# Optimization experiments

Measured on AMD Instinct MI355X. Metric: run time of the kernel, lower is better.

Reference implementation:

```python
import math
import jax, jax.numpy as jnp
import numpy as np

N = 100000
F_IN = 256
H = 64
D = 16          # dim_latent
C = 8           # n_classes
L = 10          # radial_layers
K = 10          # APPNP steps
ALPHA = 0.1
BETA_PRIOR = 0.001
E = 3200000
BN_EPS = 1e-5
LOG_SCALE = 0.5 * D * math.log(4 * math.pi)


def setup_inputs() -> dict:
    key = jax.random.key(0)
    ks = jax.random.split(key, 16)
    x = jax.random.normal(ks[0], (N, F_IN), dtype=jnp.float32)
    edge_index = jax.random.randint(ks[1], (2, E), 0, N, dtype=jnp.int64)
    s1 = 1.0 / math.sqrt(F_IN)
    s2 = 1.0 / math.sqrt(H)
    return {
        'x': x,
        'edge_index': edge_index,
        'W1': jax.random.uniform(ks[2], (F_IN, H), jnp.float32, -s1, s1),
        'b1': jnp.zeros((H,), jnp.float32),
        'g1': jnp.ones((H,), jnp.float32),
        'be1': jnp.zeros((H,), jnp.float32),
        'W2': jax.random.uniform(ks[3], (H, H), jnp.float32, -s2, s2),
        'b2': jnp.zeros((H,), jnp.float32),
        'g2': jnp.ones((H,), jnp.float32),
        'be2': jnp.zeros((H,), jnp.float32),
        'W3': jax.random.uniform(ks[4], (H, D), jnp.float32, -s2, s2),
        'b3': jnp.zeros((D,), jnp.float32),
        # flow params: per layer l, per class c
        'x0': jax.random.normal(ks[5], (L, C, D), jnp.float32) * 0.1,
        'alpha_prime': jnp.zeros((L, C), jnp.float32),
        'beta_prime': jnp.zeros((L, C), jnp.float32),
        'mu': jnp.zeros((C, D), jnp.float32),
        'log_var': jnp.zeros((C, D), jnp.float32),
    }


def _batchnorm(h, g, b):
    m = h.mean(axis=0)
    v = h.var(axis=0)  # biased, as torch BN training forward
    return g * (h - m) / jnp.sqrt(v + BN_EPS) + b


def _flow_log_prob(z, x0, alpha_prime, beta_prime, mu, log_var):
    # z: [N, D] -> log q(z|c): [N, C]. Dropout off (eval); loop over L=10 layers.
    zz = jnp.broadcast_to(z[:, None, :], (z.shape[0], C, D))  # [N,C,D]
    log_det = jnp.zeros((z.shape[0], C), z.dtype)
    for l in reversed(range(L)):  # reversed(transforms)
        a = jax.nn.softplus(alpha_prime[l])[None, :, None]      # [1,C,1]
        b = -a + jax.nn.softplus(beta_prime[l])[None, :, None]
        diff = zz - x0[l][None]                                  # [N,C,D]
        r = jnp.maximum(jnp.linalg.norm(diff, axis=-1, keepdims=True), 1e-8)
        h = 1.0 / (a + r)
        zz = zz + b * h * diff
        h_prime = -1.0 / (a + r) ** 2
        log_det = log_det + (D - 1) * jnp.log1p(b * h)[..., 0] \
                  + jnp.log1p(b * h + b * h_prime * r)[..., 0]
    var = jnp.exp(log_var)  # [C,D]
    log_p_base = (-0.5 * D * math.log(2 * math.pi)
                  - 0.5 * log_var.sum(axis=-1)[None, :]
                  - 0.5 * ((zz - mu[None]) ** 2 / var[None]).sum(axis=-1))
    return log_p_base + log_det  # [N,C]


def _appnp(beta_ft, row, col, n_nodes):
    e = row.shape[0]
    deg = jax.ops.segment_sum(jnp.ones((e,), beta_ft.dtype), row, num_segments=n_nodes)
    dis = jnp.where(deg > 0, deg ** -0.5, 0.0)
    norm = dis[row] * dis[col]  # [E']
    h = beta_ft
    for _ in range(K):
        msg = jax.ops.segment_sum(norm[:, None] * h[col], row, num_segments=n_nodes)
        h = (1.0 - ALPHA) * msg + ALPHA * beta_ft
    return h


def reference(x, edge_index, W1, b1, g1, be1, W2, b2, g2, be2, W3, b3,
              x0, alpha_prime, beta_prime, mu, log_var):
    n = x.shape[0]
    # encoder (BN in batch-stats mode, dropout disabled)
    h1 = jax.nn.relu(_batchnorm(x @ W1 + b1, g1, be1))
    h2 = jax.nn.relu(_batchnorm(h1 @ W2 + b2, g2, be2))
    z = h2 @ W3 + b3  # [N,D]
    log_q = _flow_log_prob(z, x0, alpha_prime, beta_prime, mu, log_var)  # [N,C]
    beta_ft = jnp.exp(jnp.clip(log_q + LOG_SCALE, -30.0, 30.0))
    # add self loops
    sl = jnp.arange(n, dtype=edge_index.dtype)
    row = jnp.concatenate([edge_index[0], sl])
    col = jnp.concatenate([edge_index[1], sl])
    beta_agg = _appnp(beta_ft, row, col, n)
    alpha = BETA_PRIOR + jnp.maximum(beta_agg, 0.0)
    probs = alpha / alpha.sum(axis=-1, keepdims=True)
    return alpha, probs, z, beta_ft, log_q
```

## Files before the change

kernel.cpp:

```cpp
#include <hip/hip_runtime.h>

#define NFEAT_IN 256
#define HDIM 64
#define DLAT 16
#define NC 8
#define NL 10
#define KPROP 10
#define ELLW 64
#define OVF_CAP 8192
#define NB 128
#define PERTHREAD 16
#define TILE (256 * PERTHREAD)
#define BM 64
#define BKT 64

__device__ __forceinline__ float softplusf(float x) {
    return (x > 20.f) ? x : log1pf(expf(x));
}

__global__ __launch_bounds__(256) void k_gemm1(
        const float* __restrict__ x, const float* __restrict__ W1,
        const float* __restrict__ b1, float* __restrict__ t1t, int n) {
    __shared__ float xs[BKT][BM + 4];
    __shared__ float ws[BKT][HDIM];
    int t = threadIdx.x;
    int row0 = blockIdx.x * BM;
    int tr = t >> 4, tc = t & 15;
    float acc[4][4];
    float4 bv = *reinterpret_cast<const float4*>(&b1[tc * 4]);
    #pragma unroll
    for (int i = 0; i < 4; ++i) {
        acc[i][0] = bv.x; acc[i][1] = bv.y; acc[i][2] = bv.z; acc[i][3] = bv.w;
    }
    for (int k0 = 0; k0 < NFEAT_IN; k0 += BKT) {
        __syncthreads();
        #pragma unroll
        for (int it = 0; it < 4; ++it) {
            int i = it * 256 + t;
            int row = i >> 4, q = i & 15;
            int grow = row0 + row;
            float4 v = make_float4(0.f, 0.f, 0.f, 0.f);
            if (grow < n)
                v = *reinterpret_cast<const float4*>(
                        &x[(size_t)grow * NFEAT_IN + k0 + q * 4]);
            xs[q * 4 + 0][row] = v.x;
            xs[q * 4 + 1][row] = v.y;
            xs[q * 4 + 2][row] = v.z;
            xs[q * 4 + 3][row] = v.w;
        }
        #pragma unroll
        for (int it = 0; it < 4; ++it) {
            int i = it * 256 + t;
            int kk = i >> 4, q = i & 15;
            *reinterpret_cast<float4*>(&ws[kk][q * 4]) =
                *reinterpret_cast<const float4*>(&W1[(size_t)(k0 + kk) * HDIM + q * 4]);
        }
        __syncthreads();
        #pragma unroll 8
        for (int kk = 0; kk < BKT; ++kk) {
            float4 a = *reinterpret_cast<const float4*>(&xs[kk][tr * 4]);
            float4 w = *reinterpret_cast<const float4*>(&ws[kk][tc * 4]);
            acc[0][0] += a.x * w.x; acc[0][1] += a.x * w.y;
            acc[0][2] += a.x * w.z; acc[0][3] += a.x * w.w;
            acc[1][0] += a.y * w.x; acc[1][1] += a.y * w.y;
            acc[1][2] += a.y * w.z; acc[1][3] += a.y * w.w;
            acc[2][0] += a.z * w.x; acc[2][1] += a.z * w.y;
            acc[2][2] += a.z * w.z; acc[2][3] += a.z * w.w;
            acc[3][0] += a.w * w.x; acc[3][1] += a.w * w.y;
            acc[3][2] += a.w * w.z; acc[3][3] += a.w * w.w;
        }
    }
    int r = row0 + tr * 4;
    if (r < n) {
        #pragma unroll
        for (int cj = 0; cj < 4; ++cj) {
            int j = tc * 4 + cj;
            float4 v = make_float4(acc[0][cj], acc[1][cj], acc[2][cj], acc[3][cj]);
            *reinterpret_cast<float4*>(&t1t[(size_t)j * n + r]) = v;
        }
    }
}

__global__ __launch_bounds__(256) void k_gemm2(
        const float* __restrict__ t1t, const float* __restrict__ A1,
        const float* __restrict__ B1, const float* __restrict__ W2,
        const float* __restrict__ b2, float* __restrict__ t2t, int n) {
    __shared__ float xs[HDIM][BM + 4];
    __shared__ float ws[HDIM][HDIM];
    __shared__ float As[HDIM], Bs[HDIM];
    int t = threadIdx.x;
    int row0 = blockIdx.x * BM;
    if (t < HDIM) { As[t] = A1[t]; Bs[t] = B1[t]; }
    __syncthreads();
    int tr = t >> 4, tc = t & 15;
    #pragma unroll
    for (int it = 0; it < 4; ++it) {
        int i = it * 256 + t;
        int kk = i >> 4, q = i & 15;
        float4 v = make_float4(0.f, 0.f, 0.f, 0.f);
        if (row0 + q * 4 < n) {
            v = *reinterpret_cast<const float4*>(&t1t[(size_t)kk * n + row0 + q * 4]);
            float a = As[kk], b = Bs[kk];
            v.x = fmaxf(fmaf(a, v.x, b), 0.f);
            v.y = fmaxf(fmaf(a, v.y, b), 0.f);
            v.z = fmaxf(fmaf(a, v.z, b), 0.f);
            v.w = fmaxf(fmaf(a, v.w, b), 0.f);
        }
        *reinterpret_cast<float4*>(&xs[kk][q * 4]) = v;
    }
    #pragma unroll
    for (int it = 0; it < 4; ++it) {
        int i = it * 256 + t;
        int kk = i >> 4, q = i & 15;
        *reinterpret_cast<float4*>(&ws[kk][q * 4]) =
            *reinterpret_cast<const float4*>(&W2[(size_t)kk * HDIM + q * 4]);
    }
    __syncthreads();
    float acc[4][4];
    float4 bv = *reinterpret_cast<const float4*>(&b2[tc * 4]);
    #pragma unroll
    for (int i = 0; i < 4; ++i) {
        acc[i][0] = bv.x; acc[i][1] = bv.y; acc[i][2] = bv.z; acc[i][3] = bv.w;
    }
    #pragma unroll 8
    for (int kk = 0; kk < HDIM; ++kk) {
        float4 a = *reinterpret_cast<const float4*>(&xs[kk][tr * 4]);
        float4 w = *reinterpret_cast<const float4*>(&ws[kk][tc * 4]);
        acc[0][0] += a.x * w.x; acc[0][1] += a.x * w.y;
        acc[0][2] += a.x * w.z; acc[0][3] += a.x * w.w;
        acc[1][0] += a.y * w.x; acc[1][1] += a.y * w.y;
        acc[1][2] += a.y * w.z; acc[1][3] += a.y * w.w;
        acc[2][0] += a.z * w.x; acc[2][1] += a.z * w.y;
        acc[2][2] += a.z * w.z; acc[2][3] += a.z * w.w;
        acc[3][0] += a.w * w.x; acc[3][1] += a.w * w.y;
        acc[3][2] += a.w * w.z; acc[3][3] += a.w * w.w;
    }
    int r = row0 + tr * 4;
    if (r < n) {
        #pragma unroll
        for (int cj = 0; cj < 4; ++cj) {
            int j = tc * 4 + cj;
            float4 v = make_float4(acc[0][cj], acc[1][cj], acc[2][cj], acc[3][cj]);
            *reinterpret_cast<float4*>(&t2t[(size_t)j * n + r]) = v;
        }
    }
}

__global__ __launch_bounds__(256) void k_stats(
        const float* __restrict__ tt, float* __restrict__ sum,
        float* __restrict__ sq, int n) {
    int feat = blockIdx.x >> 3;
    int chunk = blockIdx.x & 7;
    const float4* p = reinterpret_cast<const float4*>(tt + (size_t)feat * n);
    int n4 = n / 4;
    float s = 0.f, q = 0.f;
    for (int i = chunk * 256 + threadIdx.x; i < n4; i += 8 * 256) {
        float4 v = p[i];
        s += v.x + v.y + v.z + v.w;
        q += v.x * v.x + v.y * v.y + v.z * v.z + v.w * v.w;
    }
    if (chunk == 0 && threadIdx.x < (n & 3)) {
        float v = tt[(size_t)feat * n + (n & ~3) + threadIdx.x];
        s += v; q += v * v;
    }
    #pragma unroll
    for (int off = 32; off; off >>= 1) {
        s += __shfl_down(s, off, 64);
        q += __shfl_down(q, off, 64);
    }
    __shared__ float ls[4], lq[4];
    int wid = threadIdx.x >> 6, lane = threadIdx.x & 63;
    if (lane == 0) { ls[wid] = s; lq[wid] = q; }
    __syncthreads();
    if (threadIdx.x == 0) {
        atomicAdd(&sum[feat], ls[0] + ls[1] + ls[2] + ls[3]);
        atomicAdd(&sq[feat],  lq[0] + lq[1] + lq[2] + lq[3]);
    }
}

__global__ void k_finalize(const float* __restrict__ sum, const float* __restrict__ sq,
        const float* __restrict__ g, const float* __restrict__ be,
        float* __restrict__ A, float* __restrict__ B, int n) {
    int j = threadIdx.x;
    if (j >= HDIM) return;
    float mean = sum[j] / (float)n;
    float var = sq[j] / (float)n - mean * mean;
    float istd = 1.0f / sqrtf(var + 1e-5f);
    A[j] = g[j] * istd;
    B[j] = be[j] - mean * istd * g[j];
}

__global__ __launch_bounds__(256) void k_zlin(
        const float* __restrict__ t2t, const float* __restrict__ A2,
        const float* __restrict__ B2, const float* __restrict__ W3,
        const float* __restrict__ b3, float* __restrict__ out_z, int n) {
    __shared__ float As[HDIM], Bs[HDIM], Ws[HDIM * DLAT];
    int t = threadIdx.x;
    if (t < HDIM) { As[t] = A2[t]; Bs[t] = B2[t]; }
    for (int i = t; i < HDIM * DLAT; i += 256) Ws[i] = W3[i];
    __syncthreads();
    int row = blockIdx.x * 256 + t;
    if (row >= n) return;
    float z[DLAT];
    #pragma unroll
    for (int j = 0; j < DLAT; ++j) z[j] = b3[j];
    for (int k = 0; k < HDIM; ++k) {
        float hv = fmaxf(fmaf(As[k], t2t[(size_t)k * n + row], Bs[k]), 0.f);
        const float* w = &Ws[k * DLAT];
        #pragma unroll
        for (int j = 0; j < DLAT; ++j) z[j] = fmaf(hv, w[j], z[j]);
    }
    float4* zp = reinterpret_cast<float4*>(&out_z[(size_t)row * DLAT]);
    zp[0] = make_float4(z[0], z[1], z[2], z[3]);
    zp[1] = make_float4(z[4], z[5], z[6], z[7]);
    zp[2] = make_float4(z[8], z[9], z[10], z[11]);
    zp[3] = make_float4(z[12], z[13], z[14], z[15]);
}

__global__ __launch_bounds__(256) void k_flow(
        const float* __restrict__ zbuf, const float* __restrict__ x0,
        const float* __restrict__ ap, const float* __restrict__ bp,
        const float* __restrict__ mu, const float* __restrict__ lv,
        float* __restrict__ out_logq, float* __restrict__ out_beta, int n) {
    __shared__ float a_s[NL * NC], b_s[NL * NC];
    __shared__ float x0_s[NL * NC][DLAT + 1];
    __shared__ float mu_s[NC][DLAT + 1], iv_s[NC][DLAT + 1], slv_s[NC];
    int t = threadIdx.x;
    for (int i = t; i < NL * NC; i += 256) {
        float a = softplusf(ap[i]);
        a_s[i] = a;
        b_s[i] = softplusf(bp[i]) - a;
    }
    for (int i = t; i < NL * NC * DLAT; i += 256) x0_s[i >> 4][i & 15] = x0[i];
    for (int i = t; i < NC * DLAT; i += 256) {
        mu_s[i >> 4][i & 15] = mu[i];
        iv_s[i >> 4][i & 15] = __expf(-lv[i]);
    }
    if (t < NC) {
        float s = 0.f;
        for (int d = 0; d < DLAT; ++d) s += lv[t * DLAT + d];
        slv_s[t] = s;
    }
    __syncthreads();
    int gid = blockIdx.x * 256 + t;
    int row = gid >> 3, c = gid & 7;
    if (row >= n) return;
    float zz[DLAT];
    const float4* zp = reinterpret_cast<const float4*>(&zbuf[(size_t)row * DLAT]);
    float4 z0 = zp[0], z1 = zp[1], z2 = zp[2], z3 = zp[3];
    zz[0] = z0.x; zz[1] = z0.y; zz[2] = z0.z; zz[3] = z0.w;
    zz[4] = z1.x; zz[5] = z1.y; zz[6] = z1.z; zz[7] = z1.w;
    zz[8] = z2.x; zz[9] = z2.y; zz[10] = z2.z; zz[11] = z2.w;
    zz[12] = z3.x; zz[13] = z3.y; zz[14] = z3.z; zz[15] = z3.w;

    float log_det = 0.f;
    #pragma unroll
    for (int l = NL - 1; l >= 0; --l) {
        int idx = l * NC + c;
        float a = a_s[idx], b = b_s[idx];
        const float* x0p = x0_s[idx];
        float diff[DLAT];
        float r2 = 0.f;
        #pragma unroll
        for (int d = 0; d < DLAT; ++d) {
            diff[d] = zz[d] - x0p[d];
            r2 = fmaf(diff[d], diff[d], r2);
        }
        float r = fmaxf(sqrtf(r2), 1e-8f);
        float h = 1.f / (a + r);
        float bh = b * h;
        #pragma unroll
        for (int d = 0; d < DLAT; ++d) zz[d] = fmaf(bh, diff[d], zz[d]);
        log_det += (DLAT - 1) * __logf(1.f + bh) + __logf(1.f + bh - bh * h * r);
    }
    float quad = 0.f;
    #pragma unroll
    for (int d = 0; d < DLAT; ++d) {
        float dd = zz[d] - mu_s[c][d];
        quad = fmaf(dd * dd, iv_s[c][d], quad);
    }
    float lq = -14.70301653f - 0.5f * slv_s[c] - 0.5f * quad + log_det;
    out_logq[gid] = lq;
    float w = fminf(fmaxf(lq + 20.24819398f, -30.f), 30.f);
    out_beta[gid] = __expf(w);
}

__global__ __launch_bounds__(256) void k_bucket(
        const int* __restrict__ rows, const int* __restrict__ cols,
        int2* __restrict__ bpairs, int* __restrict__ bcnt, int cap,
        int* __restrict__ cur, int2* __restrict__ ovf, int* __restrict__ ovf_cnt,
        int e, int n, int rpb) {
    __shared__ int lcnt[NB], loff[NB], lcur[NB], gbase[NB], sc[NB];
    __shared__ int2 staged[TILE];
    int t = threadIdx.x;
    int base = blockIdx.x * TILE;
    for (int i = t; i < NB; i += 256) lcnt[i] = 0;
    __syncthreads();
    int er[PERTHREAD], ec[PERTHREAD], eb[PERTHREAD];
    #pragma unroll
    for (int k = 0; k < PERTHREAD; ++k) {
        int i = base + k * 256 + t;
        eb[k] = -1;
        if (i < e) {
            int r = rows[i], c = cols[i];
            if ((unsigned)r < (unsigned)n && (unsigned)c < (unsigned)n) {
                er[k] = r; ec[k] = c;
                int b = (int)((unsigned)r / (unsigned)rpb);
                eb[k] = b;
                atomicAdd(&lcnt[b], 1);
            }
        }
    }
    __syncthreads();
    if (t < NB) sc[t] = lcnt[t];
    __syncthreads();
    for (int off = 1; off < NB; off <<= 1) {
        int v = 0;
        if (t < NB && t >= off) v = sc[t - off];
        __syncthreads();
        if (t < NB) sc[t] += v;
        __syncthreads();
    }
    if (t < NB) { loff[t] = sc[t] - lcnt[t]; lcur[t] = sc[t] - lcnt[t]; }
    __syncthreads();
    #pragma unroll
    for (int k = 0; k < PERTHREAD; ++k) {
        if (eb[k] >= 0) {
            int slot = atomicAdd(&lcur[eb[k]], 1);
            staged[slot] = make_int2(er[k], ec[k]);
        }
    }
    __syncthreads();
    if (t < NB && lcnt[t] > 0) gbase[t] = atomicAdd(&bcnt[t], lcnt[t]);
    __syncthreads();
    int wid = t >> 6, lane = t & 63;
    for (int b = wid; b < NB; b += 4) {
        int cnt = lcnt[b];
        if (!cnt) continue;
        int gb = gbase[b], lo = loff[b];
        for (int k = lane; k < cnt; k += 64) {
            int2 p = staged[lo + k];
            int dst = gb + k;
            if (dst < cap) {
                bpairs[(size_t)b * cap + dst] = p;
            } else {
                int o = atomicAdd(ovf_cnt, 1);
                if (o < OVF_CAP) ovf[o] = p;
                atomicAdd(&cur[p.x], 1);
            }
        }
    }
}

__global__ __launch_bounds__(256) void k_build(
        const int2* __restrict__ bpairs, const int* __restrict__ bcnt, int cap,
        int* __restrict__ ecol, int* __restrict__ cur,
        int2* __restrict__ ovf, int* __restrict__ ovf_cnt, int n, int rpb) {
    __shared__ int lcnt[1024];
    int b = blockIdx.x, t = threadIdx.x;
    int row_base = b * rpb;
    int nrows = n - row_base; if (nrows > rpb) nrows = rpb;
    if (nrows <= 0) return;
    for (int i = t; i < nrows; i += 256) lcnt[i] = 0;
    __syncthreads();
    int m = bcnt[b]; if (m > cap) m = cap;
    const int2* bp = bpairs + (size_t)b * cap;
    for (int i = t; i < m; i += 256) {
        int2 p = bp[i];
        int lr = p.x - row_base;
        int j = atomicAdd(&lcnt[lr], 1);
        if (j < ELLW) {
            ecol[(size_t)p.x * ELLW + j] = p.y;
        } else {
            int o = atomicAdd(ovf_cnt, 1);
            if (o < OVF_CAP) ovf[o] = p;
        }
    }
    __syncthreads();
    for (int i = t; i < nrows; i += 256) {
        int c = lcnt[i];
        if (c) cur[row_base + i] += c;
    }
}

__global__ void k_dis(const int* __restrict__ cur, float* __restrict__ dis, int n) {
    int i = blockIdx.x * blockDim.x + threadIdx.x;
    if (i < n) dis[i] = rsqrtf((float)cur[i] + 1.0f);
}

__global__ void k_init_hs(const float* __restrict__ beta, const float* __restrict__ dis,
                          float* __restrict__ hs, int n) {
    int i = blockIdx.x * blockDim.x + threadIdx.x;
    if (i >= n) return;
    float d = dis[i];
    const float4* b = reinterpret_cast<const float4*>(beta + (size_t)i * NC);
    float4* o = reinterpret_cast<float4*>(hs + (size_t)i * NC);
    float4 b0 = b[0], b1 = b[1];
    o[0] = make_float4(d * b0.x, d * b0.y, d * b0.z, d * b0.w);
    o[1] = make_float4(d * b1.x, d * b1.y, d * b1.z, d * b1.w);
}

__global__ __launch_bounds__(256) void k_gather(
        const int* __restrict__ cur, const int* __restrict__ ecol,
        const float* __restrict__ hs_in, const float* __restrict__ beta,
        const float* __restrict__ dis, float* __restrict__ hout,
        float* __restrict__ hs_out, const int2* __restrict__ ovf,
        const int* __restrict__ ovf_cnt, int n) {
    int row = (blockIdx.x * blockDim.x + threadIdx.x) >> 3;
    int c = threadIdx.x & 7;
    if (row >= n) return;
    int cnt = cur[row];
    int lim = cnt < ELLW ? cnt : ELLW;
    float d = dis[row];
    const int* ec = ecol + (size_t)row * ELLW;
    const int4* ec4 = reinterpret_cast<const int4*>(ec);
    float acc = hs_in[row * NC + c];
    float a0 = 0.f, a1 = 0.f, a2 = 0.f, a3 = 0.f;
    int lim4 = lim & ~3;
    for (int ep = 0; ep < lim4; ep += 4) {
        int4 e4 = ec4[ep >> 2];
        a0 += hs_in[e4.x * NC + c];
        a1 += hs_in[e4.y * NC + c];
        a2 += hs_in[e4.z * NC + c];
        a3 += hs_in[e4.w * NC + c];
    }
    for (int ep = lim4; ep < lim; ++ep) acc += hs_in[ec[ep] * NC + c];
    acc += (a0 + a1) + (a2 + a3);
    int m = *ovf_cnt;
    if (m > 0) {
        if (m > OVF_CAP) m = OVF_CAP;
        for (int i = 0; i < m; ++i) {
            int2 p = ovf[i];
            if (p.x == row) acc += hs_in[p.y * NC + c];
        }
    }
    float hn = 0.9f * d * acc + 0.1f * beta[row * NC + c];
    hout[row * NC + c] = hn;
    hs_out[row * NC + c] = d * hn;
}

__global__ void k_final(const float* __restrict__ h, float* __restrict__ out_alpha,
        float* __restrict__ out_probs, int n) {
    int i = blockIdx.x * blockDim.x + threadIdx.x;
    if (i >= n) return;
    float a[NC];
    float s = 0.f;
    #pragma unroll
    for (int c = 0; c < NC; ++c) {
        float v = h[(size_t)i * NC + c];
        v = 0.001f + fmaxf(v, 0.f);
        a[c] = v; s += v;
    }
    float inv = 1.f / s;
    #pragma unroll
    for (int c = 0; c < NC; ++c) {
        out_alpha[(size_t)i * NC + c] = a[c];
        out_probs[(size_t)i * NC + c] = a[c] * inv;
    }
}

extern "C" void kernel_launch(void* const* d_in, const int* in_sizes, int n_in,
                              void* d_out, int out_size, void* d_ws, size_t ws_size,
                              hipStream_t stream) {
    const float* x   = (const float*)d_in[0];
    const int*   ei  = (const int*)d_in[1];
    const float* W1  = (const float*)d_in[2];
    const float* b1  = (const float*)d_in[3];
    const float* g1  = (const float*)d_in[4];
    const float* be1 = (const float*)d_in[5];
    const float* W2  = (const float*)d_in[6];
    const float* b2  = (const float*)d_in[7];
    const float* g2  = (const float*)d_in[8];
    const float* be2 = (const float*)d_in[9];
    const float* W3  = (const float*)d_in[10];
    const float* b3  = (const float*)d_in[11];
    const float* x0  = (const float*)d_in[12];
    const float* ap  = (const float*)d_in[13];
    const float* bp  = (const float*)d_in[14];
    const float* mu  = (const float*)d_in[15];
    const float* lv  = (const float*)d_in[16];

    int n = in_sizes[0] / NFEAT_IN;
    int e = in_sizes[1] / 2;
    const int* rows = ei;
    const int* cols = ei + e;
    int rpb = (n + NB - 1) / NB;
    int cap = (e + e / 16) / NB;

    size_t an = (size_t)HDIM * n;
    float* ws  = (float*)d_ws;
    float* t1t = ws;
    float* t2t = ws + an;
    int2*  bpairs = (int2*)t2t;
    float* stats = (float*)((char*)t2t + (size_t)NB * cap * sizeof(int2));
    float *sum1 = stats,       *sq1 = stats + 64,  *A1 = stats + 128, *B1 = stats + 192;
    float *sum2 = stats + 256, *sq2 = stats + 320, *A2 = stats + 384, *B2 = stats + 448;
    int*  bcnt    = (int*)(stats + 512);
    int*  ovf_cnt = bcnt + NB;
    int2* ovf     = (int2*)(ovf_cnt + 4);
    float* hs0 = (float*)bpairs;
    float* hs1 = hs0 + (size_t)NC * n;
    int* ecol = (int*)t1t;

    float* out = (float*)d_out;
    float* out_alpha = out;
    float* out_probs = out + (size_t)n * NC;
    float* out_z     = out + (size_t)2 * n * NC;
    float* out_beta  = out_z + (size_t)n * DLAT;
    float* out_logq  = out_beta + (size_t)n * NC;

    int*   cur = (int*)out_probs;
    float* dis = out_probs + n;

    int nb_nodes = (n + 255) / 256;
    int nb_gemm  = (n + BM - 1) / BM;
    int nb_nc    = (int)(((size_t)n * NC + 255) / 256);

    hipMemsetAsync(stats, 0, (512 + NB + 4) * sizeof(float), stream);

    k_gemm1<<<nb_gemm, 256, 0, stream>>>(x, W1, b1, t1t, n);
    k_stats<<<HDIM * 8, 256, 0, stream>>>(t1t, sum1, sq1, n);
    k_finalize<<<1, 64, 0, stream>>>(sum1, sq1, g1, be1, A1, B1, n);
    k_gemm2<<<nb_gemm, 256, 0, stream>>>(t1t, A1, B1, W2, b2, t2t, n);
    k_stats<<<HDIM * 8, 256, 0, stream>>>(t2t, sum2, sq2, n);
    k_finalize<<<1, 64, 0, stream>>>(sum2, sq2, g2, be2, A2, B2, n);
    k_zlin<<<nb_nodes, 256, 0, stream>>>(t2t, A2, B2, W3, b3, out_z, n);
    k_flow<<<nb_nc, 256, 0, stream>>>(out_z, x0, ap, bp, mu, lv,
                                      out_logq, out_beta, n);

    hipMemsetAsync(cur, 0, (size_t)n * sizeof(int), stream);
    int nt_bucket = (e + TILE - 1) / TILE;
    k_bucket<<<nt_bucket, 256, 0, stream>>>(rows, cols, bpairs, bcnt, cap,
                                            cur, ovf, ovf_cnt, e, n, rpb);
    k_build<<<NB, 256, 0, stream>>>(bpairs, bcnt, cap, ecol, cur, ovf, ovf_cnt, n, rpb);
    k_dis<<<nb_nodes, 256, 0, stream>>>(cur, dis, n);
    k_init_hs<<<nb_nodes, 256, 0, stream>>>(out_beta, dis, hs0, n);

    for (int it = 0; it < KPROP; ++it) {
        const float* hin = (it & 1) ? hs1 : hs0;
        float* hso = (it & 1) ? hs0 : hs1;
        k_gather<<<nb_nc, 256, 0, stream>>>(cur, ecol, hin, out_beta, dis,
                                            out_alpha, hso, ovf, ovf_cnt, n);
    }
    k_final<<<nb_nodes, 256, 0, stream>>>(out_alpha, out_alpha, out_probs, n);
}
```

Baseline: 528.1 us.

## Shrink GEMM K-tiles, store x row-major in LDS, unroll gather by eight

GEMM1 now uses a K-tile of 32 and stores x tiles row-major in shared memory with float4 writes, replacing the transposed scalar stores. GEMM2 is split into two K-tiles of 32 to reduce LDS footprint and raise occupancy. The APPNP gather loop is unrolled to eight independent accumulators to expose more memory-level parallelism. In exchange there are more barriers per block, and the scalar LDS reads in GEMM1's inner loop may cause bank conflicts.

Result: no change. 518.9 us (-1.7%).

```diff
diff --git a/kernel.cpp b/kernel.cpp
--- a/kernel.cpp
+++ b/kernel.cpp
@@ -12,7 +12,7 @@
 #define PERTHREAD 16
 #define TILE (256 * PERTHREAD)
 #define BM 64
-#define BKT 64
+#define BK1 32
 
 __device__ __forceinline__ float softplusf(float x) {
     return (x > 20.f) ? x : log1pf(expf(x));
@@ -21,8 +21,8 @@
 __global__ __launch_bounds__(256) void k_gemm1(
         const float* __restrict__ x, const float* __restrict__ W1,
         const float* __restrict__ b1, float* __restrict__ t1t, int n) {
-    __shared__ float xs[BKT][BM + 4];
-    __shared__ float ws[BKT][HDIM];
+    __shared__ float xs[BM][BK1 + 4];
+    __shared__ float ws[BK1][HDIM];
     int t = threadIdx.x;
     int row0 = blockIdx.x * BM;
     int tr = t >> 4, tc = t & 15;
@@ -32,24 +32,21 @@
     for (int i = 0; i < 4; ++i) {
         acc[i][0] = bv.x; acc[i][1] = bv.y; acc[i][2] = bv.z; acc[i][3] = bv.w;
     }
-    for (int k0 = 0; k0 < NFEAT_IN; k0 += BKT) {
+    for (int k0 = 0; k0 < NFEAT_IN; k0 += BK1) {
         __syncthreads();
         #pragma unroll
-        for (int it = 0; it < 4; ++it) {
+        for (int it = 0; it < 2; ++it) {
             int i = it * 256 + t;
-            int row = i >> 4, q = i & 15;
+            int row = i >> 3, q = i & 7;
             int grow = row0 + row;
             float4 v = make_float4(0.f, 0.f, 0.f, 0.f);
             if (grow < n)
                 v = *reinterpret_cast<const float4*>(
                         &x[(size_t)grow * NFEAT_IN + k0 + q * 4]);
-            xs[q * 4 + 0][row] = v.x;
-            xs[q * 4 + 1][row] = v.y;
-            xs[q * 4 + 2][row] = v.z;
-            xs[q * 4 + 3][row] = v.w;
-        }
-        #pragma unroll
-        for (int it = 0; it < 4; ++it) {
+            *reinterpret_cast<float4*>(&xs[row][q * 4]) = v;
+        }
+        #pragma unroll
+        for (int it = 0; it < 2; ++it) {
             int i = it * 256 + t;
             int kk = i >> 4, q = i & 15;
             *reinterpret_cast<float4*>(&ws[kk][q * 4]) =
@@ -57,17 +54,20 @@
         }
         __syncthreads();
         #pragma unroll 8
-        for (int kk = 0; kk < BKT; ++kk) {
-            float4 a = *reinterpret_cast<const float4*>(&xs[kk][tr * 4]);
+        for (int kk = 0; kk < BK1; ++kk) {
+            float a0 = xs[tr * 4 + 0][kk];
+            float a1 = xs[tr * 4 + 1][kk];
+            float a2 = xs[tr * 4 + 2][kk];
+            float a3 = xs[tr * 4 + 3][kk];
             float4 w = *reinterpret_cast<const float4*>(&ws[kk][tc * 4]);
-            acc[0][0] += a.x * w.x; acc[0][1] += a.x * w.y;
-            acc[0][2] += a.x * w.z; acc[0][3] += a.x * w.w;
-            acc[1][0] += a.y * w.x; acc[1][1] += a.y * w.y;
-            acc[1][2] += a.y * w.z; acc[1][3] += a.y * w.w;
-            acc[2][0] += a.z * w.x; acc[2][1] += a.z * w.y;
-            acc[2][2] += a.z * w.z; acc[2][3] += a.z * w.w;
-            acc[3][0] += a.w * w.x; acc[3][1] += a.w * w.y;
-            acc[3][2] += a.w * w.z; acc[3][3] += a.w * w.w;
+            acc[0][0] = fmaf(a0, w.x, acc[0][0]); acc[0][1] = fmaf(a0, w.y, acc[0][1]);
+            acc[0][2] = fmaf(a0, w.z, acc[0][2]); acc[0][3] = fmaf(a0, w.w, acc[0][3]);
+            acc[1][0] = fmaf(a1, w.x, acc[1][0]); acc[1][1] = fmaf(a1, w.y, acc[1][1]);
+            acc[1][2] = fmaf(a1, w.z, acc[1][2]); acc[1][3] = fmaf(a1, w.w, acc[1][3]);
+            acc[2][0] = fmaf(a2, w.x, acc[2][0]); acc[2][1] = fmaf(a2, w.y, acc[2][1]);
+            acc[2][2] = fmaf(a2, w.z, acc[2][2]); acc[2][3] = fmaf(a2, w.w, acc[2][3]);
+            acc[3][0] = fmaf(a3, w.x, acc[3][0]); acc[3][1] = fmaf(a3, w.y, acc[3][1]);
+            acc[3][2] = fmaf(a3, w.z, acc[3][2]); acc[3][3] = fmaf(a3, w.w, acc[3][3]);
         }
     }
     int r = row0 + tr * 4;
@@ -85,55 +85,58 @@
         const float* __restrict__ t1t, const float* __restrict__ A1,
         const float* __restrict__ B1, const float* __restrict__ W2,
         const float* __restrict__ b2, float* __restrict__ t2t, int n) {
-    __shared__ float xs[HDIM][BM + 4];
-    __shared__ float ws[HDIM][HDIM];
+    __shared__ float xs[BK1][BM + 4];
+    __shared__ float ws[BK1][HDIM];
     __shared__ float As[HDIM], Bs[HDIM];
     int t = threadIdx.x;
     int row0 = blockIdx.x * BM;
     if (t < HDIM) { As[t] = A1[t]; Bs[t] = B1[t]; }
-    __syncthreads();
     int tr = t >> 4, tc = t & 15;
-    #pragma unroll
-    for (int it = 0; it < 4; ++it) {
-        int i = it * 256 + t;
-        int kk = i >> 4, q = i & 15;
-        float4 v = make_float4(0.f, 0.f, 0.f, 0.f);
-        if (row0 + q * 4 < n) {
-            v = *reinterpret_cast<const float4*>(&t1t[(size_t)kk * n + row0 + q * 4]);
-            float a = As[kk], b = Bs[kk];
-            v.x = fmaxf(fmaf(a, v.x, b), 0.f);
-            v.y = fmaxf(fmaf(a, v.y, b), 0.f);
-            v.z = fmaxf(fmaf(a, v.z, b), 0.f);
-            v.w = fmaxf(fmaf(a, v.w, b), 0.f);
-        }
-        *reinterpret_cast<float4*>(&xs[kk][q * 4]) = v;
-    }
-    #pragma unroll
-    for (int it = 0; it < 4; ++it) {
-        int i = it * 256 + t;
-        int kk = i >> 4, q = i & 15;
-        *reinterpret_cast<float4*>(&ws[kk][q * 4]) =
-            *reinterpret_cast<const float4*>(&W2[(size_t)kk * HDIM + q * 4]);
-    }
-    __syncthreads();
     float acc[4][4];
     float4 bv = *reinterpret_cast<const float4*>(&b2[tc * 4]);
     #pragma unroll
     for (int i = 0; i < 4; ++i) {
         acc[i][0] = bv.x; acc[i][1] = bv.y; acc[i][2] = bv.z; acc[i][3] = bv.w;
     }
-    #pragma unroll 8
-    for (int kk = 0; kk < HDIM; ++kk) {
-        float4 a = *reinterpret_cast<const float4*>(&xs[kk][tr * 4]);
-        float4 w = *reinterpret_cast<const float4*>(&ws[kk][tc * 4]);
-        acc[0][0] += a.x * w.x; acc[0][1] += a.x * w.y;
-        acc[0][2] += a.x * w.z; acc[0][3] += a.x * w.w;
-        acc[1][0] += a.y * w.x; acc[1][1] += a.y * w.y;
-        acc[1][2] += a.y * w.z; acc[1][3] += a.y * w.w;
-        acc[2][0] += a.z * w.x; acc[2][1] += a.z * w.y;
-        acc[2][2] += a.z * w.z; acc[2][3] += a.z * w.w;
-        acc[3][0] += a.w * w.x; acc[3][1] += a.w * w.y;
-        acc[3][2] += a.w * w.z; acc[3][3] += a.w * w.w;
+    for (int k0 = 0; k0 < HDIM; k0 += BK1) {
+        __syncthreads();
+        #pragma unroll
+        for (int it = 0; it < 2; ++it) {
+            int i = it * 256 + t;
+            int kk = i >> 4, q = i & 15;
+            float4 v = make_float4(0.f, 0.f, 0.f, 0.f);
+            if (row0 + q * 4 < n) {
+                v = *reinterpret_cast<const float4*>(
+                        &t1t[(size_t)(k0 + kk) * n + row0 + q * 4]);
+                float a = As[k0 + kk], b = Bs[k0 + kk];
+                v.x = fmaxf(fmaf(a, v.x, b), 0.f);
+                v.y = fmaxf(fmaf(a, v.y, b), 0.f);
+                v.z = fmaxf(fmaf(a, v.z, b), 0.f);
+                v.w = fmaxf(fmaf(a, v.w, b), 0.f);
+            }
+            *reinterpret_cast<float4*>(&xs[kk][q * 4]) = v;
+        }
+        #pragma unroll
+        for (int it = 0; it < 2; ++it) {
+            int i = it * 256 + t;
+            int kk = i >> 4, q = i & 15;
+            *reinterpret_cast<float4*>(&ws[kk][q * 4]) =
+                *reinterpret_cast<const float4*>(&W2[(size_t)(k0 + kk) * HDIM + q * 4]);
+        }
+        __syncthreads();
+        #pragma unroll 8
+        for (int kk = 0; kk < BK1; ++kk) {
+            float4 a = *reinterpret_cast<const float4*>(&xs[kk][tr * 4]);
+            float4 w = *reinterpret_cast<const float4*>(&ws[kk][tc * 4]);
+            acc[0][0] = fmaf(a.x, w.x, acc[0][0]); acc[0][1] = fmaf(a.x, w.y, acc[0][1]);
+            acc[0][2] = fmaf(a.x, w.z, acc[0][2]); acc[0][3] = fmaf(a.x, w.w, acc[0][3]);
+            acc[1][0] = fmaf(a.y, w.x, acc[1][0]); acc[1][1] = fmaf(a.y, w.y, acc[1][1]);
+            acc[1][2] = fmaf(a.y, w.z, acc[1][2]); acc[1][3] = fmaf(a.y, w.w, acc[1][3]);
+            acc[2][0] = fmaf(a.z, w.x, acc[2][0]); acc[2][1] = fmaf(a.z, w.y, acc[2][1]);
+            acc[2][2] = fmaf(a.z, w.z, acc[2][2]); acc[2][3] = fmaf(a.z, w.w, acc[2][3]);
+            acc[3][0] = fmaf(a.w, w.x, acc[3][0]); acc[3][1] = fmaf(a.w, w.y, acc[3][1]);
+            acc[3][2] = fmaf(a.w, w.z, acc[3][2]); acc[3][3] = fmaf(a.w, w.w, acc[3][3]);
+        }
     }
     int r = row0 + tr * 4;
     if (r < n) {
@@ -415,17 +418,23 @@
     const int* ec = ecol + (size_t)row * ELLW;
     const int4* ec4 = reinterpret_cast<const int4*>(ec);
     float acc = hs_in[row * NC + c];
-    float a0 = 0.f, a1 = 0.f, a2 = 0.f, a3 = 0.f;
-    int lim4 = lim & ~3;
-    for (int ep = 0; ep < lim4; ep += 4) {
-        int4 e4 = ec4[ep >> 2];
-        a0 += hs_in[e4.x * NC + c];
-        a1 += hs_in[e4.y * NC + c];
-        a2 += hs_in[e4.z * NC + c];
-        a3 += hs_in[e4.w * NC + c];
-    }
-    for (int ep = lim4; ep < lim; ++ep) acc += hs_in[ec[ep] * NC + c];
-    acc += (a0 + a1) + (a2 + a3);
+    float s0 = 0.f, s1 = 0.f, s2 = 0.f, s3 = 0.f;
+    float s4 = 0.f, s5 = 0.f, s6 = 0.f, s7 = 0.f;
+    int lim8 = lim & ~7;
+    for (int ep = 0; ep < lim8; ep += 8) {
+        int4 e0 = ec4[(ep >> 2) + 0];
+        int4 e1 = ec4[(ep >> 2) + 1];
+        s0 += hs_in[e0.x * NC + c];
+        s1 += hs_in[e0.y * NC + c];
+        s2 += hs_in[e0.z * NC + c];
+        s3 += hs_in[e0.w * NC + c];
+        s4 += hs_in[e1.x * NC + c];
+        s5 += hs_in[e1.y * NC + c];
+        s6 += hs_in[e1.z * NC + c];
+        s7 += hs_in[e1.w * NC + c];
+    }
+    for (int ep = lim8; ep < lim; ++ep) acc += hs_in[ec[ep] * NC + c];
+    acc += ((s0 + s1) + (s2 + s3)) + ((s4 + s5) + (s6 + s7));
     int m = *ovf_cnt;
     if (m > 0) {
         if (m > OVF_CAP) m = OVF_CAP;
```
